# Kernel tuning notes

Measured on AMD Instinct MI355X. Metric: run time of the kernel, lower is better.

Reference implementation:

```python
import jax, jax.numpy as jnp
import numpy as np


def setup_inputs() -> dict:
    key = jax.random.key(0)
    ks = jax.random.split(key, 8)
    B, S, Ta, D = 64, 512, 8, 768
    return {
        "memory": jax.random.normal(ks[0], (B, S, D), dtype=jnp.float32),
        "aspect_states": jax.random.normal(ks[1], (B, Ta, D), dtype=jnp.float32),
        "input_ids": jnp.ones((B, S), dtype=jnp.int64),
        "input_t_ids": jnp.ones((B, Ta), dtype=jnp.int64),
        "W1": jax.random.normal(ks[2], (3 * D, D), dtype=jnp.float32) * 0.02,
        "b1": jnp.zeros((D,), dtype=jnp.float32),
        "w2": jax.random.normal(ks[3], (D,), dtype=jnp.float32) * 0.02,
        "Wm": jax.random.normal(ks[4], (D, D), dtype=jnp.float32) * 0.02,
        "bm": jnp.zeros((D,), dtype=jnp.float32),
        "Wd": jax.random.normal(ks[5], (D, 3), dtype=jnp.float32) * 0.02,
        "bd": jnp.zeros((3,), dtype=jnp.float32),
    }


def reference(memory, aspect_states, input_ids, input_t_ids, W1, b1, w2, Wm, bm, Wd, bd):
    B, S, D = memory.shape
    memory_len = jnp.sum(input_ids != 0, axis=-1)          # [B]
    aspect_len = jnp.sum(input_t_ids != 0, axis=-1)        # [B]

    # v_a: mean-pooled aspect representation  [B, D]
    v_a = jnp.sum(aspect_states, axis=1) / aspect_len.astype(memory.dtype)[:, None]
    # v_s: mean-pooled sentence representation [B, D]
    v_s = jnp.sum(memory, axis=1) / memory_len.astype(memory.dtype)[:, None]

    # locationed_memory: memory[i, idx] *= 1 - idx/memory_len[i] for idx < memory_len[i]
    idx = jnp.arange(S, dtype=memory.dtype)                 # [S]
    mlen = memory_len.astype(memory.dtype)[:, None]         # [B, 1]
    loc = jnp.where(idx[None, :] < mlen, 1.0 - idx[None, :] / mlen, 1.0)  # [B, S]
    memory = memory * loc[:, :, None]

    # chunked linear1/linear2 scorer, vectorized:
    # c_t = w2 . tanh(W1 @ [m_t ; v_a ; v_s] + b1)
    W1_m, W1_a, W1_s = W1[:D], W1[D:2 * D], W1[2 * D:]
    ctx = v_a @ W1_a + v_s @ W1_s + b1                      # [B, D]
    h = jnp.tanh(jnp.einsum("bsd,de->bse", memory, W1_m) + ctx[:, None, :])
    scores = h @ w2                                         # [B, S]
    alpha = jax.nn.softmax(scores, axis=1)

    v_ts = jnp.einsum("bsd,bs->bd", memory, alpha)          # [B, D]
    v_ns = v_ts + v_s
    v_ms = jnp.tanh(v_ns @ Wm + bm)
    logits = v_ms @ Wd + bd                                 # [B, 3]
    return logits
```

## Files before the change

kernel.cpp:

```cpp
#include <hip/hip_runtime.h>
#include <hip/hip_bf16.h>


#define NB 64
#define NS 512
#define ND 768
#define NTA 8

typedef __attribute__((ext_vector_type(8))) __bf16 bf16x8;
typedef __attribute__((ext_vector_type(4))) float f32x4;

#define OFF_SCORES 0u
#define OFF_VS 131072u
#define OFF_VTS 327680u
#define OFF_CTX 524288u
#define OFF_U 720896u
#define ZERO_BYTES 917504u
#define OFF_VA 917504u
#define OFF_ALPHA 1114112u
#define OFF_LENS 1245184u
#define OFF_W1MT 1246208u
#define OFF_MP 2425856u

__device__ __forceinline__ float fast_tanh(float x) {
  x = fminf(fmaxf(x, -15.f), 15.f);
  float t = __expf(2.f * x);
  return __fdividef(t - 1.f, t + 1.f);
}

__device__ __forceinline__ unsigned bfpack2(float a, float b) {
  unsigned ua = __float_as_uint(a), ub = __float_as_uint(b);
  ua = (ua + 0x7FFFu + ((ua >> 16) & 1u)) >> 16;
  ub = (ub + 0x7FFFu + ((ub >> 16) & 1u)) >> 16;
  return ua | (ub << 16);
}

__device__ __forceinline__ unsigned short bf16b(float f) {
  unsigned u = __float_as_uint(f);
  u = (u + 0x7FFFu + ((u >> 16) & 1u)) >> 16;
  return (unsigned short)u;
}

__device__ __forceinline__ void async_copy16(const void* g, void* l) {
  __builtin_amdgcn_global_load_lds(
      (const __attribute__((address_space(1))) void*)g,
      (__attribute__((address_space(3))) void*)l, 16, 0, 0);
}

__global__ __launch_bounds__(128) void k_prep(const int* __restrict__ ids,
                                              const int* __restrict__ tids,
                                              const float* __restrict__ aspect,
                                              float* __restrict__ v_a,
                                              float* __restrict__ lens) {
  int b = blockIdx.x, tid = threadIdx.x;
  __shared__ int red[128];
  __shared__ float sh_inva;
  int cnt = 0;
  for (int j = tid; j < NS; j += 128) cnt += (ids[b * NS + j] != 0);
  red[tid] = cnt;
  __syncthreads();
  for (int s = 64; s > 0; s >>= 1) {
    if (tid < s) red[tid] += red[tid + s];
    __syncthreads();
  }
  if (tid == 0) {
    int mlen = red[0];
    int acnt = 0;
    for (int t = 0; t < NTA; ++t) acnt += (tids[b * NTA + t] != 0);
    lens[b] = (float)mlen;
    lens[64 + b] = 1.0f / (float)mlen;
    float inva = 1.0f / (float)acnt;
    lens[128 + b] = inva;
    sh_inva = inva;
  }
  __syncthreads();
  float inva = sh_inva;
  for (int j = tid; j < ND; j += 128) {
    float s = 0.f;
    for (int t = 0; t < NTA; ++t) s += aspect[((size_t)b * NTA + t) * ND + j];
    v_a[b * ND + j] = s * inva;
  }
}

__global__ __launch_bounds__(192) void k_vs_mprime(const float* __restrict__ memory,
                                                   const float* __restrict__ lens,
                                                   float* __restrict__ v_s,
                                                   unsigned short* __restrict__ mp) {
  int sc = blockIdx.x, b = blockIdx.y, tid = threadIdx.x;
  int d0 = tid * 4;
  float inv_mlen = lens[64 + b];
  float mlenf = lens[b];
  float s0 = 0, s1 = 0, s2 = 0, s3 = 0;
#pragma unroll 4
  for (int s = 0; s < 32; ++s) {
    int srow = sc * 32 + s;
    size_t row = (size_t)b * NS + srow;
    const float4 v = *(const float4*)(memory + row * ND + d0);
    s0 += v.x; s1 += v.y; s2 += v.z; s3 += v.w;
    float fs = (float)srow;
    float loc = (fs < mlenf) ? 1.0f - fs * inv_mlen : 1.0f;
    uint2 pk;
    pk.x = bfpack2(v.x * loc, v.y * loc);
    pk.y = bfpack2(v.z * loc, v.w * loc);
    *(uint2*)(mp + row * ND + d0) = pk;
  }
  float* p = v_s + b * ND + d0;
  atomicAdd(p + 0, s0 * inv_mlen);
  atomicAdd(p + 1, s1 * inv_mlen);
  atomicAdd(p + 2, s2 * inv_mlen);
  atomicAdd(p + 3, s3 * inv_mlen);
}

__global__ __launch_bounds__(256) void k_transpose(const float* __restrict__ W1,
                                                   unsigned short* __restrict__ w1mt) {
  __shared__ float tile[32][33];
  int bx = blockIdx.x, by = blockIdx.y;
  int tx = threadIdx.x, ty = threadIdx.y;
  for (int j = 0; j < 32; j += 8)
    tile[ty + j][tx] = W1[(size_t)(by * 32 + ty + j) * ND + bx * 32 + tx];
  __syncthreads();
  for (int j = 0; j < 32; j += 8)
    w1mt[(size_t)(bx * 32 + ty + j) * ND + by * 32 + tx] = bf16b(tile[tx][ty + j]);
}

__global__ __launch_bounds__(128) void k_ctx(const float* __restrict__ W1,
                                             const float* __restrict__ v_a,
                                             const float* __restrict__ v_s,
                                             float* __restrict__ ctx) {
  int et = blockIdx.x, b = blockIdx.y, dc = blockIdx.z, tid = threadIdx.x;
  __shared__ float vbuf[384];
  for (int j = tid; j < 384; j += 128) {
    int k = dc * 384 + j;
    vbuf[j] = (k < ND) ? v_a[b * ND + k] : v_s[b * ND + (k - ND)];
  }
  __syncthreads();
  int e = et * 128 + tid;
  float acc = 0.f;
  const float* Wk = W1 + (size_t)(ND + dc * 384) * ND + e;
#pragma unroll 8
  for (int j = 0; j < 384; ++j) acc += vbuf[j] * Wk[(size_t)j * ND];
  atomicAdd(&ctx[b * ND + e], acc);
}

__global__ __launch_bounds__(256) void k_gemm_scores(const unsigned short* __restrict__ mp,
                                                     const unsigned short* __restrict__ w1mt,
                                                     const float* __restrict__ ctx,
                                                     const float* __restrict__ b1,
                                                     const float* __restrict__ w2,
                                                     float* __restrict__ scores) {
  __shared__ char lds[65536];
  const int tid = threadIdx.x;
  const int wave = tid >> 6, lane = tid & 63;
  const int bid = blockIdx.x;
  const int swz = (bid & 7) * 192 + (bid >> 3);
  const int rt = swz / 6;
  const int et = swz - rt * 6;
  const int row0 = rt * 128, n0 = et * 128;
  const int b = row0 >> 9;
  const int wm = wave & 1, wn = wave >> 1;

  const int lrow = lane >> 3;
  const int qlog = (lane & 7) ^ lrow;
  const char* Abase = (const char*)mp + (size_t)(row0 + lrow) * (ND * 2) + qlog * 16;
  const char* Bbase = (const char*)w1mt + (size_t)(n0 + lrow) * (ND * 2) + qlog * 16;

  f32x4 acc[4][4];
#pragma unroll
  for (int i = 0; i < 4; ++i)
#pragma unroll
    for (int t = 0; t < 4; ++t) acc[i][t] = (f32x4){0.f, 0.f, 0.f, 0.f};

  const int q2 = lane >> 4, c = lane & 15;
  int offA[4][2], offB[4][2];
#pragma unroll
  for (int i = 0; i < 4; ++i) {
    int ml = wm * 64 + i * 16 + c;
    offA[i][0] = ml * 128 + ((q2 ^ (ml & 7)) * 16);
    offA[i][1] = ml * 128 + (((4 + q2) ^ (ml & 7)) * 16);
    int nl = wn * 64 + i * 16 + c;
    offB[i][0] = nl * 128 + ((q2 ^ (nl & 7)) * 16);
    offB[i][1] = nl * 128 + (((4 + q2) ^ (nl & 7)) * 16);
  }

  auto stage = [&](int bufsel, int kb) {
    char* lA = lds + bufsel * 32768;
    char* lB = lA + 16384;
#pragma unroll
    for (int i = 0; i < 4; ++i) {
      int g = wave * 4 + i;
      async_copy16(Abase + (size_t)g * 8 * (ND * 2) + kb, lA + g * 1024);
      async_copy16(Bbase + (size_t)g * 8 * (ND * 2) + kb, lB + g * 1024);
    }
  };

  stage(0, 0);
  __syncthreads();

  int cur = 0;
#pragma unroll 2
  for (int t = 0; t < 12; ++t) {
    if (t < 11) stage(cur ^ 1, (t + 1) * 128);
    const char* lA = lds + cur * 32768;
    const char* lB = lA + 16384;
    bf16x8 af[2][4], bfr[2][4];
#pragma unroll
    for (int kk = 0; kk < 2; ++kk)
#pragma unroll
      for (int i = 0; i < 4; ++i) {
        af[kk][i] = *(const bf16x8*)(lA + offA[i][kk]);
        bfr[kk][i] = *(const bf16x8*)(lB + offB[i][kk]);
      }
#pragma unroll
    for (int kk = 0; kk < 2; ++kk)
#pragma unroll
      for (int i = 0; i < 4; ++i)
#pragma unroll
        for (int t2 = 0; t2 < 4; ++t2)
          acc[i][t2] = __builtin_amdgcn_mfma_f32_16x16x32_bf16(af[kk][i], bfr[kk][t2], acc[i][t2], 0, 0, 0);
    __syncthreads();
    cur ^= 1;
  }

  float ctxv[4], w2v[4];
#pragma unroll
  for (int t = 0; t < 4; ++t) {
    int n = n0 + wn * 64 + t * 16 + c;
    ctxv[t] = ctx[b * ND + n] + b1[n];
    w2v[t] = w2[n];
  }
#pragma unroll
  for (int i = 0; i < 4; ++i) {
#pragma unroll
    for (int r = 0; r < 4; ++r) {
      float s = 0.f;
#pragma unroll
      for (int t = 0; t < 4; ++t) s += fast_tanh(acc[i][t][r] + ctxv[t]) * w2v[t];
      s += __shfl_xor(s, 1, 64);
      s += __shfl_xor(s, 2, 64);
      s += __shfl_xor(s, 4, 64);
      s += __shfl_xor(s, 8, 64);
      if (c == 0) atomicAdd(&scores[row0 + wm * 64 + i * 16 + q2 * 4 + r], s);
    }
  }
}

__global__ __launch_bounds__(512) void k_softmax(const float* __restrict__ scores,
                                                 float* __restrict__ alpha) {
  int b = blockIdx.x, tid = threadIdx.x;
  int wid = tid >> 6, lane = tid & 63;
  __shared__ float red[8], red2[8];
  float v = scores[b * NS + tid];
  float m = v;
  for (int off = 1; off < 64; off <<= 1) m = fmaxf(m, __shfl_xor(m, off, 64));
  if (lane == 0) red[wid] = m;
  __syncthreads();
  if (tid == 0) {
    float mm = red[0];
    for (int i = 1; i < 8; ++i) mm = fmaxf(mm, red[i]);
    red[0] = mm;
  }
  __syncthreads();
  float M = red[0];
  float e = __expf(v - M);
  float s = e;
  for (int off = 1; off < 64; off <<= 1) s += __shfl_xor(s, off, 64);
  if (lane == 0) red2[wid] = s;
  __syncthreads();
  if (tid == 0) {
    float ss = 0.f;
    for (int i = 0; i < 8; ++i) ss += red2[i];
    red2[0] = ss;
  }
  __syncthreads();
  alpha[b * NS + tid] = e / red2[0];
}

__global__ __launch_bounds__(192) void k_vts(const unsigned short* __restrict__ mp,
                                             const float* __restrict__ alpha,
                                             float* __restrict__ v_ts) {
  int sc = blockIdx.x, b = blockIdx.y, tid = threadIdx.x;
  __shared__ float al[32];
  if (tid < 32) al[tid] = alpha[b * NS + sc * 32 + tid];
  __syncthreads();
  int d0 = tid * 4;
  float a0 = 0, a1 = 0, a2 = 0, a3 = 0;
#pragma unroll 4
  for (int s = 0; s < 32; ++s) {
    size_t row = (size_t)b * NS + sc * 32 + s;
    uint2 pk = *(const uint2*)(mp + row * ND + d0);
    float a = al[s];
    a0 += a * __uint_as_float(pk.x << 16);
    a1 += a * __uint_as_float(pk.x & 0xFFFF0000u);
    a2 += a * __uint_as_float(pk.y << 16);
    a3 += a * __uint_as_float(pk.y & 0xFFFF0000u);
  }
  float* p = v_ts + b * ND + d0;
  atomicAdd(p + 0, a0);
  atomicAdd(p + 1, a1);
  atomicAdd(p + 2, a2);
  atomicAdd(p + 3, a3);
}

__global__ __launch_bounds__(128) void k_final1(const float* __restrict__ v_ts,
                                                const float* __restrict__ v_s,
                                                const float* __restrict__ Wm,
                                                float* __restrict__ u) {
  int et = blockIdx.x, b = blockIdx.y, dc = blockIdx.z, tid = threadIdx.x;
  __shared__ float vbuf[192];
  for (int j = tid; j < 192; j += 128) {
    int d = dc * 192 + j;
    vbuf[j] = v_ts[b * ND + d] + v_s[b * ND + d];
  }
  __syncthreads();
  int e = et * 128 + tid;
  float acc = 0.f;
  const float* Wk = Wm + (size_t)(dc * 192) * ND + e;
#pragma unroll 8
  for (int j = 0; j < 192; ++j) acc += vbuf[j] * Wk[(size_t)j * ND];
  atomicAdd(&u[b * ND + e], acc);
}

__global__ __launch_bounds__(256) void k_final2(const float* __restrict__ u,
                                                const float* __restrict__ bm,
                                                const float* __restrict__ Wd,
                                                const float* __restrict__ bd,
                                                float* __restrict__ out) {
  int b = blockIdx.x, tid = threadIdx.x;
  int wid = tid >> 6, lane = tid & 63;
  __shared__ float red[4][3];
  float p0 = 0, p1 = 0, p2 = 0;
  for (int e = tid; e < ND; e += 256) {
    float vm = fast_tanh(u[b * ND + e] + bm[e]);
    p0 += vm * Wd[e * 3 + 0];
    p1 += vm * Wd[e * 3 + 1];
    p2 += vm * Wd[e * 3 + 2];
  }
  for (int off = 1; off < 64; off <<= 1) {
    p0 += __shfl_xor(p0, off, 64);
    p1 += __shfl_xor(p1, off, 64);
    p2 += __shfl_xor(p2, off, 64);
  }
  if (lane == 0) { red[wid][0] = p0; red[wid][1] = p1; red[wid][2] = p2; }
  __syncthreads();
  if (tid == 0) {
    out[b * 3 + 0] = red[0][0] + red[1][0] + red[2][0] + red[3][0] + bd[0];
    out[b * 3 + 1] = red[0][1] + red[1][1] + red[2][1] + red[3][1] + bd[1];
    out[b * 3 + 2] = red[0][2] + red[1][2] + red[2][2] + red[3][2] + bd[2];
  }
}

extern "C" void kernel_launch(void* const* d_in, const int* in_sizes, int n_in,
                              void* d_out, int out_size, void* d_ws, size_t ws_size,
                              hipStream_t stream) {
  const float* memory = (const float*)d_in[0];
  const float* aspect = (const float*)d_in[1];
  const int* ids = (const int*)d_in[2];
  const int* tids = (const int*)d_in[3];
  const float* W1 = (const float*)d_in[4];
  const float* b1 = (const float*)d_in[5];
  const float* w2 = (const float*)d_in[6];
  const float* Wm = (const float*)d_in[7];
  const float* bm = (const float*)d_in[8];
  const float* Wd = (const float*)d_in[9];
  const float* bd = (const float*)d_in[10];
  float* out = (float*)d_out;

  char* ws = (char*)d_ws;
  float* scores = (float*)(ws + OFF_SCORES);
  float* v_s = (float*)(ws + OFF_VS);
  float* v_ts = (float*)(ws + OFF_VTS);
  float* ctx = (float*)(ws + OFF_CTX);
  float* u = (float*)(ws + OFF_U);
  float* v_a = (float*)(ws + OFF_VA);
  float* alpha = (float*)(ws + OFF_ALPHA);
  float* lens = (float*)(ws + OFF_LENS);
  unsigned short* w1mt = (unsigned short*)(ws + OFF_W1MT);
  unsigned short* mp = (unsigned short*)(ws + OFF_MP);

  hipMemsetAsync(ws, 0, ZERO_BYTES, stream);

  k_prep<<<NB, 128, 0, stream>>>(ids, tids, aspect, v_a, lens);
  k_transpose<<<dim3(24, 24), dim3(32, 8), 0, stream>>>(W1, w1mt);
  k_vs_mprime<<<dim3(16, NB), 192, 0, stream>>>(memory, lens, v_s, mp);
  k_ctx<<<dim3(6, NB, 4), 128, 0, stream>>>(W1, v_a, v_s, ctx);
  k_gemm_scores<<<1536, 256, 0, stream>>>(mp, w1mt, ctx, b1, w2, scores);
  k_softmax<<<NB, 512, 0, stream>>>(scores, alpha);
  k_vts<<<dim3(16, NB), 192, 0, stream>>>(mp, alpha, v_ts);
  k_final1<<<dim3(6, NB, 4), 128, 0, stream>>>(v_ts, v_s, Wm, u);
  k_final2<<<NB, 256, 0, stream>>>(u, bm, Wd, bd, out);
}
```

Baseline: 322.4 us.

## Fuse prep/transpose, softmax into vts, final stages; deepen GEMM LDS pipeline

Merges the W1 transpose and the length/aspect prep into one launch. Folds the softmax into k_vts, with each block recomputing the row max and sum from scores, and folds the two final matvec kernels into a single per-batch kernel. In the scores GEMM, the double-buffered loop now prefetches two stages ahead, uses explicit waitcnt and barriers, and raises priority around the MFMAs. These changes cut launch count and intermediate traffic. In exchange the softmax is recomputed 16x per batch row, and the final matvec runs with only 64 blocks.

```diff
diff --git a/kernel.cpp b/kernel.cpp
--- a/kernel.cpp
+++ b/kernel.cpp
@@ -14,13 +14,11 @@
 #define OFF_VS 131072u
 #define OFF_VTS 327680u
 #define OFF_CTX 524288u
-#define OFF_U 720896u
-#define ZERO_BYTES 917504u
-#define OFF_VA 917504u
-#define OFF_ALPHA 1114112u
-#define OFF_LENS 1245184u
-#define OFF_W1MT 1246208u
-#define OFF_MP 2425856u
+#define ZERO_BYTES 720896u
+#define OFF_VA 720896u
+#define OFF_LENS 917504u
+#define OFF_W1MT 918528u
+#define OFF_MP 2098176u
 
 __device__ __forceinline__ float fast_tanh(float x) {
   x = fminf(fmaxf(x, -15.f), 15.f);
@@ -47,38 +45,52 @@
       (__attribute__((address_space(3))) void*)l, 16, 0, 0);
 }
 
-__global__ __launch_bounds__(128) void k_prep(const int* __restrict__ ids,
-                                              const int* __restrict__ tids,
-                                              const float* __restrict__ aspect,
-                                              float* __restrict__ v_a,
-                                              float* __restrict__ lens) {
-  int b = blockIdx.x, tid = threadIdx.x;
-  __shared__ int red[128];
-  __shared__ float sh_inva;
-  int cnt = 0;
-  for (int j = tid; j < NS; j += 128) cnt += (ids[b * NS + j] != 0);
-  red[tid] = cnt;
-  __syncthreads();
-  for (int s = 64; s > 0; s >>= 1) {
-    if (tid < s) red[tid] += red[tid + s];
+__global__ __launch_bounds__(256) void k_prep_tr(const int* __restrict__ ids,
+                                                 const int* __restrict__ tids,
+                                                 const float* __restrict__ aspect,
+                                                 const float* __restrict__ W1,
+                                                 float* __restrict__ v_a,
+                                                 float* __restrict__ lens,
+                                                 unsigned short* __restrict__ w1mt) {
+  int bid = blockIdx.x, tid = threadIdx.x;
+  if (bid < 576) {
+    __shared__ float tile[32][33];
+    int bx = bid % 24, by = bid / 24;
+    int tx = tid & 31, ty = tid >> 5;
+    for (int j = 0; j < 32; j += 8)
+      tile[ty + j][tx] = W1[(size_t)(by * 32 + ty + j) * ND + bx * 32 + tx];
     __syncthreads();
-  }
-  if (tid == 0) {
-    int mlen = red[0];
-    int acnt = 0;
-    for (int t = 0; t < NTA; ++t) acnt += (tids[b * NTA + t] != 0);
-    lens[b] = (float)mlen;
-    lens[64 + b] = 1.0f / (float)mlen;
-    float inva = 1.0f / (float)acnt;
-    lens[128 + b] = inva;
-    sh_inva = inva;
-  }
-  __syncthreads();
-  float inva = sh_inva;
-  for (int j = tid; j < ND; j += 128) {
-    float s = 0.f;
-    for (int t = 0; t < NTA; ++t) s += aspect[((size_t)b * NTA + t) * ND + j];
-    v_a[b * ND + j] = s * inva;
+    for (int j = 0; j < 32; j += 8)
+      w1mt[(size_t)(bx * 32 + ty + j) * ND + by * 32 + tx] = bf16b(tile[tx][ty + j]);
+  } else {
+    int b = bid - 576;
+    __shared__ int red[256];
+    __shared__ float sh_inva;
+    int cnt = 0;
+    for (int j = tid; j < NS; j += 256) cnt += (ids[b * NS + j] != 0);
+    red[tid] = cnt;
+    __syncthreads();
+    for (int s = 128; s > 0; s >>= 1) {
+      if (tid < s) red[tid] += red[tid + s];
+      __syncthreads();
+    }
+    if (tid == 0) {
+      int mlen = red[0];
+      int acnt = 0;
+      for (int t = 0; t < NTA; ++t) acnt += (tids[b * NTA + t] != 0);
+      lens[b] = (float)mlen;
+      lens[64 + b] = 1.0f / (float)mlen;
+      float inva = 1.0f / (float)acnt;
+      lens[128 + b] = inva;
+      sh_inva = inva;
+    }
+    __syncthreads();
+    float inva = sh_inva;
+    for (int j = tid; j < ND; j += 256) {
+      float s = 0.f;
+      for (int t = 0; t < NTA; ++t) s += aspect[((size_t)b * NTA + t) * ND + j];
+      v_a[b * ND + j] = s * inva;
+    }
   }
 }
 
@@ -91,7 +103,7 @@
   float inv_mlen = lens[64 + b];
   float mlenf = lens[b];
   float s0 = 0, s1 = 0, s2 = 0, s3 = 0;
-#pragma unroll 4
+#pragma unroll 8
   for (int s = 0; s < 32; ++s) {
     int srow = sc * 32 + s;
     size_t row = (size_t)b * NS + srow;
@@ -109,18 +121,6 @@
   atomicAdd(p + 1, s1 * inv_mlen);
   atomicAdd(p + 2, s2 * inv_mlen);
   atomicAdd(p + 3, s3 * inv_mlen);
-}
-
-__global__ __launch_bounds__(256) void k_transpose(const float* __restrict__ W1,
-                                                   unsigned short* __restrict__ w1mt) {
-  __shared__ float tile[32][33];
-  int bx = blockIdx.x, by = blockIdx.y;
-  int tx = threadIdx.x, ty = threadIdx.y;
-  for (int j = 0; j < 32; j += 8)
-    tile[ty + j][tx] = W1[(size_t)(by * 32 + ty + j) * ND + bx * 32 + tx];
-  __syncthreads();
-  for (int j = 0; j < 32; j += 8)
-    w1mt[(size_t)(bx * 32 + ty + j) * ND + by * 32 + tx] = bf16b(tile[tx][ty + j]);
 }
 
 __global__ __launch_bounds__(128) void k_ctx(const float* __restrict__ W1,
@@ -194,13 +194,15 @@
   };
 
   stage(0, 0);
-  __syncthreads();
-
-  int cur = 0;
-#pragma unroll 2
+  stage(1, 128);
+
+#pragma unroll
   for (int t = 0; t < 12; ++t) {
-    if (t < 11) stage(cur ^ 1, (t + 1) * 128);
-    const char* lA = lds + cur * 32768;
+    if (t < 11) { asm volatile("s_waitcnt vmcnt(8)" ::: "memory"); }
+    else        { asm volatile("s_waitcnt vmcnt(0)" ::: "memory"); }
+    __builtin_amdgcn_s_barrier();
+    __builtin_amdgcn_sched_barrier(0);
+    const char* lA = lds + (t & 1) * 32768;
     const char* lB = lA + 16384;
     bf16x8 af[2][4], bfr[2][4];
 #pragma unroll
@@ -210,6 +212,12 @@
         af[kk][i] = *(const bf16x8*)(lA + offA[i][kk]);
         bfr[kk][i] = *(const bf16x8*)(lB + offB[i][kk]);
       }
+    asm volatile("s_waitcnt lgkmcnt(0)" ::: "memory");
+    __builtin_amdgcn_sched_barrier(0);
+    __builtin_amdgcn_s_barrier();
+    if (t + 2 < 12) stage(t & 1, (t + 2) * 128);
+    __builtin_amdgcn_sched_barrier(0);
+    __builtin_amdgcn_s_setprio(1);
 #pragma unroll
     for (int kk = 0; kk < 2; ++kk)
 #pragma unroll
@@ -217,8 +225,7 @@
 #pragma unroll
         for (int t2 = 0; t2 < 4; ++t2)
           acc[i][t2] = __builtin_amdgcn_mfma_f32_16x16x32_bf16(af[kk][i], bfr[kk][t2], acc[i][t2], 0, 0, 0);
-    __syncthreads();
-    cur ^= 1;
+    __builtin_amdgcn_s_setprio(0);
   }
 
   float ctxv[4], w2v[4];
@@ -244,44 +251,29 @@
   }
 }
 
-__global__ __launch_bounds__(512) void k_softmax(const float* __restrict__ scores,
-                                                 float* __restrict__ alpha) {
-  int b = blockIdx.x, tid = threadIdx.x;
-  int wid = tid >> 6, lane = tid & 63;
-  __shared__ float red[8], red2[8];
-  float v = scores[b * NS + tid];
-  float m = v;
-  for (int off = 1; off < 64; off <<= 1) m = fmaxf(m, __shfl_xor(m, off, 64));
-  if (lane == 0) red[wid] = m;
-  __syncthreads();
-  if (tid == 0) {
-    float mm = red[0];
-    for (int i = 1; i < 8; ++i) mm = fmaxf(mm, red[i]);
-    red[0] = mm;
-  }
-  __syncthreads();
-  float M = red[0];
-  float e = __expf(v - M);
-  float s = e;
-  for (int off = 1; off < 64; off <<= 1) s += __shfl_xor(s, off, 64);
-  if (lane == 0) red2[wid] = s;
-  __syncthreads();
-  if (tid == 0) {
-    float ss = 0.f;
-    for (int i = 0; i < 8; ++i) ss += red2[i];
-    red2[0] = ss;
-  }
-  __syncthreads();
-  alpha[b * NS + tid] = e / red2[0];
-}
-
 __global__ __launch_bounds__(192) void k_vts(const unsigned short* __restrict__ mp,
-                                             const float* __restrict__ alpha,
+                                             const float* __restrict__ scores,
                                              float* __restrict__ v_ts) {
   int sc = blockIdx.x, b = blockIdx.y, tid = threadIdx.x;
+  int lane = tid & 63, wid = tid >> 6;
+  __shared__ float sred[3], sred2[3];
   __shared__ float al[32];
-  if (tid < 32) al[tid] = alpha[b * NS + sc * 32 + tid];
-  __syncthreads();
+  float v0 = scores[b * NS + tid];
+  float v1 = scores[b * NS + tid + 192];
+  float v2 = (tid < 128) ? scores[b * NS + tid + 384] : -1e30f;
+  float m = fmaxf(fmaxf(v0, v1), v2);
+  for (int off = 1; off < 64; off <<= 1) m = fmaxf(m, __shfl_xor(m, off, 64));
+  if (lane == 0) sred[wid] = m;
+  __syncthreads();
+  float M = fmaxf(fmaxf(sred[0], sred[1]), sred[2]);
+  float e = __expf(v0 - M) + __expf(v1 - M) + ((tid < 128) ? __expf(v2 - M) : 0.f);
+  for (int off = 1; off < 64; off <<= 1) e += __shfl_xor(e, off, 64);
+  if (lane == 0) sred2[wid] = e;
+  __syncthreads();
+  float invS = 1.0f / (sred2[0] + sred2[1] + sred2[2]);
+  if (tid < 32) al[tid] = __expf(scores[b * NS + sc * 32 + tid] - M) * invS;
+  __syncthreads();
+
   int d0 = tid * 4;
   float a0 = 0, a1 = 0, a2 = 0, a3 = 0;
 #pragma unroll 4
@@ -301,39 +293,40 @@
   atomicAdd(p + 3, a3);
 }
 
-__global__ __launch_bounds__(128) void k_final1(const float* __restrict__ v_ts,
-                                                const float* __restrict__ v_s,
-                                                const float* __restrict__ Wm,
-                                                float* __restrict__ u) {
-  int et = blockIdx.x, b = blockIdx.y, dc = blockIdx.z, tid = threadIdx.x;
-  __shared__ float vbuf[192];
-  for (int j = tid; j < 192; j += 128) {
-    int d = dc * 192 + j;
-    vbuf[j] = v_ts[b * ND + d] + v_s[b * ND + d];
-  }
-  __syncthreads();
-  int e = et * 128 + tid;
-  float acc = 0.f;
-  const float* Wk = Wm + (size_t)(dc * 192) * ND + e;
-#pragma unroll 8
-  for (int j = 0; j < 192; ++j) acc += vbuf[j] * Wk[(size_t)j * ND];
-  atomicAdd(&u[b * ND + e], acc);
-}
-
-__global__ __launch_bounds__(256) void k_final2(const float* __restrict__ u,
-                                                const float* __restrict__ bm,
-                                                const float* __restrict__ Wd,
-                                                const float* __restrict__ bd,
-                                                float* __restrict__ out) {
+__global__ __launch_bounds__(256) void k_final(const float* __restrict__ v_ts,
+                                               const float* __restrict__ v_s,
+                                               const float* __restrict__ Wm,
+                                               const float* __restrict__ bm,
+                                               const float* __restrict__ Wd,
+                                               const float* __restrict__ bd,
+                                               float* __restrict__ out) {
   int b = blockIdx.x, tid = threadIdx.x;
   int wid = tid >> 6, lane = tid & 63;
+  __shared__ float vb[ND];
   __shared__ float red[4][3];
+  for (int d = tid; d < ND; d += 256) vb[d] = v_ts[b * ND + d] + v_s[b * ND + d];
+  __syncthreads();
+  float a0 = 0, a1 = 0, a2 = 0;
+  const float* W0 = Wm + tid;
+#pragma unroll 4
+  for (int d = 0; d < ND; ++d) {
+    float v = vb[d];
+    const float* Wr = W0 + (size_t)d * ND;
+    a0 += v * Wr[0];
+    a1 += v * Wr[256];
+    a2 += v * Wr[512];
+  }
   float p0 = 0, p1 = 0, p2 = 0;
-  for (int e = tid; e < ND; e += 256) {
-    float vm = fast_tanh(u[b * ND + e] + bm[e]);
-    p0 += vm * Wd[e * 3 + 0];
-    p1 += vm * Wd[e * 3 + 1];
-    p2 += vm * Wd[e * 3 + 2];
+  {
+    int e = tid;
+    float vm = fast_tanh(a0 + bm[e]);
+    p0 += vm * Wd[e * 3 + 0]; p1 += vm * Wd[e * 3 + 1]; p2 += vm * Wd[e * 3 + 2];
+    e = tid + 256;
+    vm = fast_tanh(a1 + bm[e]);
+    p0 += vm * Wd[e * 3 + 0]; p1 += vm * Wd[e * 3 + 1]; p2 += vm * Wd[e * 3 + 2];
+    e = tid + 512;
+    vm = fast_tanh(a2 + bm[e]);
+    p0 += vm * Wd[e * 3 + 0]; p1 += vm * Wd[e * 3 + 1]; p2 += vm * Wd[e * 3 + 2];
   }
   for (int off = 1; off < 64; off <<= 1) {
     p0 += __shfl_xor(p0, off, 64);
@@ -370,22 +363,17 @@
   float* v_s = (float*)(ws + OFF_VS);
   float* v_ts = (float*)(ws + OFF_VTS);
   float* ctx = (float*)(ws + OFF_CTX);
-  float* u = (float*)(ws + OFF_U);
   float* v_a = (float*)(ws + OFF_VA);
-  float* alpha = (float*)(ws + OFF_ALPHA);
   float* lens = (float*)(ws + OFF_LENS);
   unsigned short* w1mt = (unsigned short*)(ws + OFF_W1MT);
   unsigned short* mp = (unsigned short*)(ws + OFF_MP);
 
   hipMemsetAsync(ws, 0, ZERO_BYTES, stream);
 
-  k_prep<<<NB, 128, 0, stream>>>(ids, tids, aspect, v_a, lens);
-  k_transpose<<<dim3(24, 24), dim3(32, 8), 0, stream>>>(W1, w1mt);
+  k_prep_tr<<<640, 256, 0, stream>>>(ids, tids, aspect, W1, v_a, lens, w1mt);
   k_vs_mprime<<<dim3(16, NB), 192, 0, stream>>>(memory, lens, v_s, mp);
   k_ctx<<<dim3(6, NB, 4), 128, 0, stream>>>(W1, v_a, v_s, ctx);
   k_gemm_scores<<<1536, 256, 0, stream>>>(mp, w1mt, ctx, b1, w2, scores);
-  k_softmax<<<NB, 512, 0, stream>>>(scores, alpha);
-  k_vts<<<dim3(16, NB), 192, 0, stream>>>(mp, alpha, v_ts);
-  k_final1<<<dim3(6, NB, 4), 128, 0, stream>>>(v_ts, v_s, Wm, u);
-  k_final2<<<NB, 256, 0, stream>>>(u, bm, Wd, bd, out);
-}
+  k_vts<<<dim3(16, NB), 192, 0, stream>>>(mp, scores, v_ts);
+  k_final<<<NB, 256, 0, stream>>>(v_ts, v_s, Wm, bm, Wd, bd, out);
+}
```

After: 384.5 us. +19.2%, slower.
